# Optimization experiments

Measured on AMD Instinct MI355X. Metric: run time of the kernel, lower is better.

Reference implementation:

```python
import jax, jax.numpy as jnp
import numpy as np

NEG_SLOPE = 0.2

def _gc(inp, adj, W, b):
    # Kipf GraphConvolution: adj @ (inp @ W) + b
    return adj @ (inp @ W) + b

def _lrelu(x):
    return jnp.where(x >= 0, x, NEG_SLOPE * x)

def setup_inputs() -> dict:
    key = jax.random.key(0)
    ks = jax.random.split(key, 24)
    Nx, Ny, Fx, Fy, D1, C = 8192, 4096, 512, 256, 256, 64
    s = 0.05
    inp = {
        "hx1": jax.random.uniform(ks[0], (Nx, Nx), jnp.float32) / Nx,
        "hx2": jax.random.uniform(ks[1], (Nx, Ny), jnp.float32) / Ny,
        "x0": jax.random.normal(ks[2], (Nx, Fx), jnp.float32),
        "hy1": jax.random.uniform(ks[3], (Ny, Ny), jnp.float32) / Ny,
        "hy2": jax.random.uniform(ks[4], (Ny, Nx), jnp.float32) / Nx,
        "y0": jax.random.normal(ks[5], (Ny, Fy), jnp.float32),
        "alpha": jnp.float32(0.6),
        "beta": jnp.float32(0.4),
        # weights/biases of the 8 GraphConvolution layers
        "Wx1a": jax.random.normal(ks[6], (Fx, D1), jnp.float32) * s,
        "bx1a": jnp.zeros((D1,), jnp.float32),
        "Wx1b": jax.random.normal(ks[7], (Fy, D1), jnp.float32) * s,
        "bx1b": jnp.zeros((D1,), jnp.float32),
        "Wx2a": jax.random.normal(ks[8], (D1, C), jnp.float32) * s,
        "bx2a": jnp.zeros((C,), jnp.float32),
        "Wx2b": jax.random.normal(ks[9], (D1, C), jnp.float32) * s,
        "bx2b": jnp.zeros((C,), jnp.float32),
        "Wy1a": jax.random.normal(ks[10], (Fy, D1), jnp.float32) * s,
        "by1a": jnp.zeros((D1,), jnp.float32),
        "Wy1b": jax.random.normal(ks[11], (Fx, D1), jnp.float32) * s,
        "by1b": jnp.zeros((D1,), jnp.float32),
        "Wy2a": jax.random.normal(ks[12], (D1, C), jnp.float32) * s,
        "by2a": jnp.zeros((C,), jnp.float32),
        "Wy2b": jax.random.normal(ks[13], (D1, C), jnp.float32) * s,
        "by2b": jnp.zeros((C,), jnp.float32),
    }
    return inp

def reference(hx1, hx2, x0, hy1, hy2, y0, alpha, beta,
              Wx1a, bx1a, Wx1b, bx1b, Wx2a, bx2a, Wx2b, bx2b,
              Wy1a, by1a, Wy1b, by1b, Wy2a, by2a, Wy2b, by2b):
    # layer 1
    x1 = _lrelu(_gc(x0, hx1, Wx1a, bx1a) * alpha + _gc(y0, hx2, Wx1b, bx1b) * (1 - alpha))
    y1 = _lrelu(_gc(y0, hy1, Wy1a, by1a) * beta + _gc(x0, hy2, Wy1b, by1b) * (1 - beta))
    # layer 2
    x2 = _lrelu(_gc(x1, hx1, Wx2a, bx2a) * alpha + _gc(y1, hx2, Wx2b, bx2b) * (1 - alpha))
    y_pre = _gc(y1, hy1, Wy2a, by2a) * beta + _gc(x1, hy2, Wy2b, by2b) * (1 - beta)
    y2 = _lrelu(y_pre)
    h_hat = jax.nn.sigmoid(x2 @ y2.T)            # [Nx, Ny]
    x_output = jax.nn.log_softmax(x2, axis=1)    # [Nx, nclass]
    return (h_hat, x_output)
```

## Files before the change

### kernel.cpp

```cpp
#include <hip/hip_runtime.h>

typedef unsigned short u16;
typedef unsigned char u8;
typedef long i64;
typedef __attribute__((ext_vector_type(8))) short bf16x8;
typedef __attribute__((ext_vector_type(4))) float f32x4;
typedef __attribute__((ext_vector_type(8))) u16 u16x8;
typedef __attribute__((ext_vector_type(4))) u16 u16x4;
typedef __attribute__((ext_vector_type(4))) float f4;

#define DEVI static __device__ __forceinline__

DEVI u16 f2b(float f) { __bf16 h = (__bf16)f; return __builtin_bit_cast(u16, h); }
DEVI float b2f(u16 h) { unsigned u = ((unsigned)h) << 16; return __builtin_bit_cast(float, u); }

DEVI int pk8(float a, float b, float c, float d) {
  int w = __builtin_amdgcn_cvt_pk_fp8_f32(a, b, 0, false);
  return __builtin_amdgcn_cvt_pk_fp8_f32(c, d, w, true);
}

DEVI void gload16(const void* g, void* l) {
  __builtin_amdgcn_global_load_lds((const __attribute__((address_space(1))) void*)g,
                                   (__attribute__((address_space(3))) void*)l, 16, 0, 0);
}

__global__ __launch_bounds__(1024)
void gemmF_k(const float* __restrict__ xA0, const float* __restrict__ xA1,
             const u8* __restrict__ xB0, const u8* __restrict__ xB1,
             u8* __restrict__ xA0f8, u8* __restrict__ xA1f8,
             int xK0, int xK1, int xL0, int xL1, u16* __restrict__ xC, size_t xMN,
             const float* __restrict__ yA0, const float* __restrict__ yA1,
             const u8* __restrict__ yB0, const u8* __restrict__ yB1,
             u8* __restrict__ yA0f8, u8* __restrict__ yA1f8,
             int yK0, int yK1, int yL0, int yL1, u16* __restrict__ yC, size_t yMN)
{
  constexpr int BM = 128, BK = 64;
  constexpr int LDA = 72;
  constexpr int ASZ = BM * LDA;
  constexpr int BSZ = 256 * BK;
  constexpr int BUFSZ = ASZ + BSZ;
  constexpr float SADJ = 8192.f;
  __shared__ __align__(16) u8 lds[4 * BUFSZ];

  const int tid = threadIdx.x, lane = tid & 63, wave = tid >> 6;
  const int wm = (wave >> 2) * 32, wn = (wave & 3) * 64;
  const int lgrp = lane >> 4, lrow = lane & 15;

  const int flat = blockIdx.x;

  const float *A0, *A1; const u8 *B0, *B1; u8 *A0f8, *A1f8;
  int K0, K1, L0, L1; u16* Cout; size_t MN; int m0, z;
  if (flat < 256) {
    const int s = ((flat & 7) << 5) | (flat >> 3);
    A0=xA0; A1=xA1; B0=xB0; B1=xB1; A0f8=xA0f8; A1f8=xA1f8;
    K0=xK0; K1=xK1; L0=xL0; L1=xL1; Cout=xC; MN=xMN;
    m0 = (s & 63) * BM; z = s >> 6;
  } else {
    const int f2 = flat - 256;
    const int s = ((f2 & 7) << 5) | (f2 >> 3);
    A0=yA0; A1=yA1; B0=yB0; B1=yB1; A0f8=yA0f8; A1f8=yA1f8;
    K0=yK0; K1=yK1; L0=yL0; L1=yL1; Cout=yC; MN=yMN;
    m0 = (s & 31) * BM; z = s >> 5;
  }

  const int nt0 = L0 >> 6, NT = nt0 + (L1 >> 6);

  const int r0 = tid >> 4;
  const int cf = (tid & 15) << 2;

  f32x4 acc[2][4];
#pragma unroll
  for (int m = 0; m < 2; ++m)
#pragma unroll
    for (int n = 0; n < 4; ++n) acc[m][n] = (f32x4){0.f, 0.f, 0.f, 0.f};

  f4 rA0[2], rA1[2];

  auto tileinfo = [&](int t, const float*& Ap, const u8*& Bp, u8*& Af8, int& Kj, int& kk) {
    if (t < nt0) { Ap = A0; Bp = B0; Af8 = A0f8; Kj = K0; kk = z * L0 + (t << 6); }
    else         { Ap = A1; Bp = B1; Af8 = A1f8; Kj = K1; kk = z * L1 + ((t - nt0) << 6); }
  };

  auto loadA = [&](int t, f4 (&r)[2]) {
    const float* Ap; const u8* Bp; u8* Af8; int Kj, kk;
    tileinfo(t, Ap, Bp, Af8, Kj, kk);
#pragma unroll
    for (int j = 0; j < 2; ++j) {
      const int rr = j * 64 + r0;
      r[j] = __builtin_nontemporal_load(
          (const f4*)(Ap + (size_t)(m0 + rr) * Kj + kk + cf));
    }
  };

  auto loadB = [&](int t) {
    const float* Ap; const u8* Bp; u8* Af8; int Kj, kk;
    tileinfo(t, Ap, Bp, Af8, Kj, kk);
    u8* sB = &lds[(t & 3) * BUFSZ] + ASZ;
    const int off = tid * 16;
    const int r = off >> 6, c = off & 63;
    gload16(Bp + (size_t)r * Kj + kk + (c ^ (((r >> 1) & 3) << 4)), sB + off);
  };

  auto writeA = [&](int t, f4 (&r)[2]) {
    const float* Ap; const u8* Bp; u8* Af8; int Kj, kk;
    tileinfo(t, Ap, Bp, Af8, Kj, kk);
    u8* sA = &lds[(t & 3) * BUFSZ];
#pragma unroll
    for (int j = 0; j < 2; ++j) {
      const int rr = j * 64 + r0;
      const int pw = pk8(r[j][0] * SADJ, r[j][1] * SADJ, r[j][2] * SADJ, r[j][3] * SADJ);
      *(int*)&sA[rr * LDA + cf] = pw;
      *(int*)(Af8 + (size_t)(m0 + rr) * Kj + kk + cf) = pw;
    }
  };

  auto compute = [&](int t) {
    const u8* sA = &lds[(t & 3) * BUFSZ];
    const u8* sB = sA + ASZ;
    __builtin_amdgcn_s_setprio(1);
#pragma unroll
    for (int ks = 0; ks < 2; ++ks) {
      i64 a[2], b[4];
#pragma unroll
      for (int m = 0; m < 2; ++m) {
        const int r = wm + m * 16 + lrow;
        a[m] = *(const i64*)&sA[r * LDA + ks * 32 + lgrp * 8];
      }
#pragma unroll
      for (int n = 0; n < 4; ++n) {
        const int r = wn + n * 16 + lrow;
        b[n] = *(const i64*)&sB[r * BK + ((ks * 32 + lgrp * 8) ^ (((r >> 1) & 3) << 4))];
      }
#pragma unroll
      for (int m = 0; m < 2; ++m)
#pragma unroll
        for (int n = 0; n < 4; ++n)
          acc[m][n] = __builtin_amdgcn_mfma_f32_16x16x32_fp8_fp8(a[m], b[n], acc[m][n], 0, 0, 0);
    }
    __builtin_amdgcn_s_setprio(0);
  };

  auto step = [&](int t, f4 (&rIn)[2], f4 (&rOut)[2]) {
    const bool has_next = (t + 1 < NT);
    if (has_next) { loadA(t + 1, rOut); loadB(t + 1); }
    if (!has_next)   asm volatile("s_waitcnt vmcnt(0)" ::: "memory");
    else if (t == 0) asm volatile("s_waitcnt vmcnt(3)" ::: "memory");
    else             asm volatile("s_waitcnt vmcnt(5)" ::: "memory");
    writeA(t, rIn);
    asm volatile("s_waitcnt lgkmcnt(0)" ::: "memory");
    asm volatile("s_barrier" ::: "memory");
    compute(t);
  };

  loadA(0, rA0); loadB(0);

  for (int t = 0; t < NT; t += 2) {
    step(t, rA0, rA1);
    step(t + 1, rA1, rA0);
  }

  u16* Cp = Cout + (size_t)z * MN;
#pragma unroll
  for (int n = 0; n < 4; ++n) {
    const int c = wn + n * 16 + lrow;
#pragma unroll
    for (int m = 0; m < 2; ++m) {
      const int rb = m0 + wm + m * 16 + lgrp * 4;
#pragma unroll
      for (int q = 0; q < 4; ++q)
        Cp[(size_t)(rb + q) * 256 + c] = f2b(acc[m][n][q]);
    }
  }
}

__global__ __launch_bounds__(256)
void gemm8_k(const u8* __restrict__ xA0, const u8* __restrict__ xA1,
             const u8* __restrict__ xB0, const u8* __restrict__ xB1,
             int xK0, int xK1, int xL0, int xL1, u16* __restrict__ xC, size_t xMN,
             const u8* __restrict__ yA0, const u8* __restrict__ yA1,
             const u8* __restrict__ yB0, const u8* __restrict__ yB1,
             int yK0, int yK1, int yL0, int yL1, u16* __restrict__ yC, size_t yMN)
{
  constexpr int BM = 128, BK = 128, BN = 64;
  constexpr int MR = 4, NR = 2;
  constexpr int ASZ = BM * BK, BSZ = BN * BK;
  __shared__ __align__(16) u8 lds[3 * (ASZ + BSZ)];

  const int tid = threadIdx.x, lane = tid & 63, wave = tid >> 6;
  const int wm = (wave >> 1) * 64, wn = (wave & 1) * 32;
  const int lgrp = lane >> 4, lrow = lane & 15;

  const int flat = blockIdx.x;

  const u8 *A0, *A1, *B0, *B1; int K0, K1, L0, L1; u16* Cw; size_t MN;
  int m0, z;
  if (flat < 512) {
    const int s = ((flat & 7) << 6) | (flat >> 3);
    A0=xA0; A1=xA1; B0=xB0; B1=xB1; K0=xK0; K1=xK1; L0=xL0; L1=xL1; Cw=xC; MN=xMN;
    m0 = (s & 63) * BM; z = s >> 6;
  } else {
    const int f2 = flat - 512;
    const int s = ((f2 & 7) << 6) | (f2 >> 3);
    A0=yA0; A1=yA1; B0=yB0; B1=yB1; K0=yK0; K1=yK1; L0=yL0; L1=yL1; Cw=yC; MN=yMN;
    m0 = (s & 31) * BM; z = s >> 5;
  }

  const int nt0 = L0 >> 7, NT = nt0 + (L1 >> 7);

  f32x4 acc[MR][NR];
#pragma unroll
  for (int m = 0; m < MR; ++m)
#pragma unroll
    for (int n = 0; n < NR; ++n) acc[m][n] = (f32x4){0.f, 0.f, 0.f, 0.f};

  auto stage = [&](int buf, int t) {
    const u8* Ap; const u8* Bp; int Kj, kk;
    if (t < nt0) { Ap = A0; Bp = B0; Kj = K0; kk = z * L0 + (t << 7); }
    else         { Ap = A1; Bp = B1; Kj = K1; kk = z * L1 + ((t - nt0) << 7); }
    u8* sA = &lds[buf * (ASZ + BSZ)];
    u8* sB = sA + ASZ;
#pragma unroll
    for (int i = 0; i < ASZ / 4096; ++i) {
      const int off = i * 4096 + tid * 16;
      const int r = off >> 7, c = off & 127;
      gload16(Ap + (size_t)(m0 + r) * Kj + kk + (c ^ ((r & 7) << 4)), sA + off);
    }
#pragma unroll
    for (int i = 0; i < BSZ / 4096; ++i) {
      const int off = i * 4096 + tid * 16;
      const int r = off >> 7, c = off & 127;
      gload16(Bp + (size_t)r * Kj + kk + (c ^ ((r & 7) << 4)), sB + off);
    }
  };

  auto compute = [&](int buf) {
    const u8* sA = &lds[buf * (ASZ + BSZ)];
    const u8* sB = sA + ASZ;
    __builtin_amdgcn_s_setprio(1);
#pragma unroll
    for (int ks = 0; ks < 4; ++ks) {
      i64 a[MR], b[NR];
#pragma unroll
      for (int m = 0; m < MR; ++m) {
        const int r = wm + m * 16 + lrow;
        a[m] = *(const i64*)&sA[r * BK + ((ks * 32 + lgrp * 8) ^ ((r & 7) << 4))];
      }
#pragma unroll
      for (int n = 0; n < NR; ++n) {
        const int r = wn + n * 16 + lrow;
        b[n] = *(const i64*)&sB[r * BK + ((ks * 32 + lgrp * 8) ^ ((r & 7) << 4))];
      }
#pragma unroll
      for (int m = 0; m < MR; ++m)
#pragma unroll
        for (int n = 0; n < NR; ++n)
          acc[m][n] = __builtin_amdgcn_mfma_f32_16x16x32_fp8_fp8(a[m], b[n], acc[m][n], 0, 0, 0);
    }
    __builtin_amdgcn_s_setprio(0);
  };

  stage(0, 0);
  stage(1, 1);
  for (int t = 0; t < NT; ++t) {
    if (t + 1 < NT) asm volatile("s_waitcnt vmcnt(6)" ::: "memory");
    else            asm volatile("s_waitcnt vmcnt(0)" ::: "memory");
    asm volatile("s_barrier" ::: "memory");
    compute(t % 3);
    if (t + 2 < NT) stage((t + 2) % 3, t + 2);
  }

  u16* Cp = Cw + (size_t)z * MN;
#pragma unroll
  for (int n = 0; n < NR; ++n) {
    const int c = wn + n * 16 + lrow;
#pragma unroll
    for (int m = 0; m < MR; ++m) {
      const int rb = m0 + wm + m * 16 + lgrp * 4;
#pragma unroll
      for (int q = 0; q < 4; ++q)
        Cp[(size_t)(rb + q) * 64 + c] = f2b(acc[m][n][q]);
    }
  }
}

template<bool A_F32>
__global__ __launch_bounds__(256)
void gemmS_k(const void* Ax, const u16* Bx, int Kx, int ldcx, u8* Cx1, u8* Cx2,
             const void* Ay, const u16* By, int Ky, int ldcy, u8* Cy1, u8* Cy2,
             int ySplit, int nsplit, float sOut)
{
  constexpr int BM = 64, BN = 64, BK = 32, LD = 40;
  constexpr int MR = 2, NR = 2;
  __shared__ u16 sA[BM * LD];
  __shared__ u16 sB[BN * LD];

  const int tid  = threadIdx.x;
  const int lane = tid & 63;
  const int wave = tid >> 6;
  const int wm = (wave >> 1) * 32;
  const int wn = (wave &  1) * 32;

  const void* A0_; const u16* B0_; int K0, ldc; u8 *C1, *C2; int m0;
  if ((int)blockIdx.y < ySplit) {
    A0_ = Ax; B0_ = Bx; K0 = Kx; ldc = ldcx; C1 = Cx1; C2 = Cx2;
    m0 = blockIdx.y * BM;
  } else {
    A0_ = Ay; B0_ = By; K0 = Ky; ldc = ldcy; C1 = Cy1; C2 = Cy2;
    m0 = (blockIdx.y - ySplit) * BM;
  }
  const int n0 = blockIdx.x * BN;

  constexpr int TPRA = 256 / BM;
  constexpr int EPTA = 32 / TPRA;
  const int ar = tid / TPRA, ac = (tid % TPRA) * EPTA;
  const int br = ar, bc = ac;

  f32x4 acc[MR][NR];
#pragma unroll
  for (int m = 0; m < MR; ++m)
#pragma unroll
    for (int n = 0; n < NR; ++n) acc[m][n] = (f32x4){0.f, 0.f, 0.f, 0.f};

  const int lgrp = lane >> 4, lrow = lane & 15;

  for (int kk = 0; kk < K0; kk += BK) {
    if constexpr (A_F32) {
      const float* Ap = (const float*)A0_ + (size_t)(m0 + ar) * K0 + kk + ac;
      f4 v0 = ((const f4*)Ap)[0];
      f4 v1 = ((const f4*)Ap)[1];
      u16x8 h;
      h[0]=f2b(v0[0]); h[1]=f2b(v0[1]); h[2]=f2b(v0[2]); h[3]=f2b(v0[3]);
      h[4]=f2b(v1[0]); h[5]=f2b(v1[1]); h[6]=f2b(v1[2]); h[7]=f2b(v1[3]);
      *(u16x8*)&sA[ar * LD + ac] = h;
    } else {
      const u16* Ap = (const u16*)A0_ + (size_t)(m0 + ar) * K0 + kk + ac;
      *(u16x8*)&sA[ar * LD + ac] = *(const u16x8*)Ap;
    }
    {
      const u16* Bp = B0_ + (size_t)(n0 + br) * K0 + kk + bc;
      *(u16x8*)&sB[br * LD + bc] = *(const u16x8*)Bp;
    }
    __syncthreads();
    bf16x8 af[MR], bfr[NR];
#pragma unroll
    for (int m = 0; m < MR; ++m)
      af[m] = *(const bf16x8*)&sA[(wm + m * 16 + lrow) * LD + lgrp * 8];
#pragma unroll
    for (int n = 0; n < NR; ++n)
      bfr[n] = *(const bf16x8*)&sB[(wn + n * 16 + lrow) * LD + lgrp * 8];
#pragma unroll
    for (int m = 0; m < MR; ++m)
#pragma unroll
      for (int n = 0; n < NR; ++n)
        acc[m][n] = __builtin_amdgcn_mfma_f32_16x16x32_bf16(af[m], bfr[n], acc[m][n], 0, 0, 0);
    __syncthreads();
  }

#pragma unroll
  for (int n = 0; n < NR; ++n) {
    const int c = n0 + wn + n * 16 + lrow;
    u8* Cp = (c < nsplit) ? C1 : C2;
    const int cr = (c < nsplit) ? c : c - nsplit;
#pragma unroll
    for (int m = 0; m < MR; ++m) {
      const int rb = m0 + wm + m * 16 + lgrp * 4;
      int w = __builtin_amdgcn_cvt_pk_fp8_f32(acc[m][n][0] * sOut, acc[m][n][1] * sOut, 0, false);
      w = __builtin_amdgcn_cvt_pk_fp8_f32(acc[m][n][2] * sOut, acc[m][n][3] * sOut, w, true);
      *(int*)&Cp[(size_t)cr * ldc + rb] = w;
    }
  }
}

__global__ __launch_bounds__(256)
void gemmH_k(const u16* A0_, const u16* B0_, int K0, float* Cout, int ldc)
{
  constexpr int BM = 128, BN = 128, BK = 32, LD = 40;
  constexpr int MR = 4, NR = 4;
  __shared__ u16 sA[BM * LD];
  __shared__ u16 sB[BN * LD];

  const int tid  = threadIdx.x;
  const int lane = tid & 63;
  const int wave = tid >> 6;
  const int wm = (wave >> 1) * 64;
  const int wn = (wave &  1) * 64;
  const int m0 = blockIdx.y * BM;
  const int n0 = blockIdx.x * BN;

  constexpr int TPRA = 2;
  constexpr int EPTA = 16;
  const int ar = tid / TPRA, ac = (tid % TPRA) * EPTA;

  f32x4 acc[MR][NR];
#pragma unroll
  for (int m = 0; m < MR; ++m)
#pragma unroll
    for (int n = 0; n < NR; ++n) acc[m][n] = (f32x4){0.f, 0.f, 0.f, 0.f};

  const int lgrp = lane >> 4, lrow = lane & 15;

  for (int kk = 0; kk < K0; kk += BK) {
    {
      const u16* Ap = A0_ + (size_t)(m0 + ar) * K0 + kk + ac;
      *(u16x8*)&sA[ar * LD + ac]     = ((const u16x8*)Ap)[0];
      *(u16x8*)&sA[ar * LD + ac + 8] = ((const u16x8*)Ap)[1];
      const u16* Bp = B0_ + (size_t)(n0 + ar) * K0 + kk + ac;
      *(u16x8*)&sB[ar * LD + ac]     = ((const u16x8*)Bp)[0];
      *(u16x8*)&sB[ar * LD + ac + 8] = ((const u16x8*)Bp)[1];
    }
    __syncthreads();
    bf16x8 af[MR], bfr[NR];
#pragma unroll
    for (int m = 0; m < MR; ++m)
      af[m] = *(const bf16x8*)&sA[(wm + m * 16 + lrow) * LD + lgrp * 8];
#pragma unroll
    for (int n = 0; n < NR; ++n)
      bfr[n] = *(const bf16x8*)&sB[(wn + n * 16 + lrow) * LD + lgrp * 8];
#pragma unroll
    for (int m = 0; m < MR; ++m)
#pragma unroll
      for (int n = 0; n < NR; ++n)
        acc[m][n] = __builtin_amdgcn_mfma_f32_16x16x32_bf16(af[m], bfr[n], acc[m][n], 0, 0, 0);
    __syncthreads();
  }

  float* Cp = Cout;
#pragma unroll
  for (int n = 0; n < NR; ++n) {
    const int c = n0 + wn + n * 16 + lrow;
#pragma unroll
    for (int m = 0; m < MR; ++m) {
      const int rb = m0 + wm + m * 16 + lgrp * 4;
#pragma unroll
      for (int q = 0; q < 4; ++q)
        __builtin_nontemporal_store(1.f / (1.f + __expf(-acc[m][n][q])),
                                    &Cp[(size_t)(rb + q) * ldc + c]);
    }
  }
}

__global__ __launch_bounds__(256)
void combine1_k(const u16* __restrict__ partX, const u16* __restrict__ partY,
                int xBlocks, size_t MNx, size_t MNy, int KSx_, int KSy_,
                const float* bxa, const float* bxb, const float* ap,
                const float* bya, const float* byb, const float* bp,
                u16* x1, u16* y1, float invs)
{
  const u16* parts; size_t MN; int KS, nb, bid = blockIdx.x;
  const float *b0, *b1, *mixp; u16* out;
  if (bid < xBlocks) {
    parts = partX; MN = MNx; KS = KSx_; b0 = bxa; b1 = bxb; mixp = ap; out = x1; nb = xBlocks;
  } else {
    bid -= xBlocks;
    parts = partY; MN = MNy; KS = KSy_; b0 = bya; b1 = byb; mixp = bp; out = y1;
    nb = gridDim.x - xBlocks;
  }
  const float mix = *mixp;
  const size_t stride = (size_t)nb * 1024;
  for (size_t i = ((size_t)bid * 256 + threadIdx.x) * 4; i < MN; i += stride) {
    f4 s = {0.f, 0.f, 0.f, 0.f};
    for (int zz = 0; zz < KS; ++zz) {
      u16x4 pv = *(const u16x4*)&parts[(size_t)zz * MN + i];
#pragma unroll
      for (int q = 0; q < 4; ++q) s[q] += b2f(pv[q]);
    }
    const int c = (int)(i & 255);
    u16x4 o;
#pragma unroll
    for (int q = 0; q < 4; ++q) {
      float v = s[q] * invs + mix * b0[c + q] + (1.f - mix) * b1[c + q];
      v = v >= 0.f ? v : 0.2f * v;
      o[q] = f2b(v);
    }
    *(u16x4*)&out[i] = o;
  }
}

__global__ __launch_bounds__(256)
void combine2_k(const u16* __restrict__ partX, const u16* __restrict__ partY,
                int xRowBlocks, size_t MNx, size_t MNy,
                const float* bxa, const float* bxb, const float* ap,
                const float* bya, const float* byb, const float* bp,
                u16* x2, u16* y2, float* xout, float invs)
{
  const int w = threadIdx.x >> 6, lane = threadIdx.x & 63;
  if ((int)blockIdx.x < xRowBlocks) {
    const int row = blockIdx.x * 4 + w;
    const float a = *ap;
    float s = 0.f;
#pragma unroll
    for (int z = 0; z < 8; ++z)
      s += b2f(partX[(size_t)z * MNx + (size_t)row * 64 + lane]);
    float v = s * invs + a * bxa[lane] + (1.f - a) * bxb[lane];
    v = v >= 0.f ? v : 0.2f * v;
    x2[(size_t)row * 64 + lane] = f2b(v);
    float m = v;
#pragma unroll
    for (int o = 32; o; o >>= 1) m = fmaxf(m, __shfl_xor(m, o));
    float t = __expf(v - m);
#pragma unroll
    for (int o = 32; o; o >>= 1) t += __shfl_xor(t, o);
    xout[(size_t)row * 64 + lane] = v - m - __logf(t);
  } else {
    const int row = ((int)blockIdx.x - xRowBlocks) * 4 + w;
    const float b = *bp;
    float s = 0.f;
#pragma unroll
    for (int z = 0; z < 16; ++z)
      s += b2f(partY[(size_t)z * MNy + (size_t)row * 64 + lane]);
    float v = s * invs + b * bya[lane] + (1.f - b) * byb[lane];
    v = v >= 0.f ? v : 0.2f * v;
    y2[(size_t)row * 64 + lane] = f2b(v);
  }
}

__global__ __launch_bounds__(256)
void prep_w(const float* Wx1a, const float* Wx1b, const float* Wy1a, const float* Wy1b,
            const float* Wx2a, const float* Wx2b, const float* Wy2a, const float* Wy2b,
            u16* WtX, u16* WtY, u16* W2X, u16* W2Y,
            const float* ap, const float* bp)
{
  const int zz = blockIdx.z;
  const float a = *ap, b = *bp;
  const float* W; u16* O; int K, N, roff; float s;
  switch (zz) {
    case 0: W=Wx1a; O=WtX; K=512; N=256; roff=0;   s=a;      break;
    case 1: W=Wy1b; O=WtX; K=512; N=256; roff=256; s=1.f-b;  break;
    case 2: W=Wx1b; O=WtY; K=256; N=256; roff=0;   s=1.f-a;  break;
    case 3: W=Wy1a; O=WtY; K=256; N=256; roff=256; s=b;      break;
    case 4: W=Wx2a; O=W2X; K=256; N=64;  roff=0;   s=a;      break;
    case 5: W=Wy2b; O=W2X; K=256; N=64;  roff=64;  s=1.f-b;  break;
    case 6: W=Wx2b; O=W2Y; K=256; N=64;  roff=0;   s=1.f-a;  break;
    default:W=Wy2a; O=W2Y; K=256; N=64;  roff=64;  s=b;      break;
  }
  const int total = K * N;
  for (int i = blockIdx.x * 256 + threadIdx.x; i < total; i += gridDim.x * 256) {
    const int k = i / N, n = i - k * N;
    O[(size_t)(n + roff) * K + k] = f2b(W[i] * s);
  }
}

extern "C" void kernel_launch(void* const* d_in, const int* in_sizes, int n_in,
                              void* d_out, int out_size, void* d_ws, size_t ws_size,
                              hipStream_t stream)
{
  const float* hx1 = (const float*)d_in[0];
  const float* hx2 = (const float*)d_in[1];
  const float* x0  = (const float*)d_in[2];
  const float* hy1 = (const float*)d_in[3];
  const float* hy2 = (const float*)d_in[4];
  const float* y0  = (const float*)d_in[5];
  const float* alphap = (const float*)d_in[6];
  const float* betap  = (const float*)d_in[7];
  const float* Wx1a = (const float*)d_in[8];  const float* bx1a = (const float*)d_in[9];
  const float* Wx1b = (const float*)d_in[10]; const float* bx1b = (const float*)d_in[11];
  const float* Wx2a = (const float*)d_in[12]; const float* bx2a = (const float*)d_in[13];
  const float* Wx2b = (const float*)d_in[14]; const float* bx2b = (const float*)d_in[15];
  const float* Wy1a = (const float*)d_in[16]; const float* by1a = (const float*)d_in[17];
  const float* Wy1b = (const float*)d_in[18]; const float* by1b = (const float*)d_in[19];
  const float* Wy2a = (const float*)d_in[20]; const float* by2a = (const float*)d_in[21];
  const float* Wy2b = (const float*)d_in[22]; const float* by2b = (const float*)d_in[23];
  (void)in_sizes; (void)n_in; (void)out_size;

  constexpr int Nx = 8192, Ny = 4096, Fx = 512, Fy = 256, D1 = 256, C = 64;
  constexpr float SB1 = 16.f, SB2 = 256.f;
  constexpr float INV1 = 1.f / (8192.f * 16.f);
  constexpr float INV2 = 1.f / (8192.f * 256.f);
  constexpr int KSx = 4, KSy = 8;

  u8* wsb = (u8*)d_ws;
  size_t off = 0;
  auto alloc = [&](size_t n) { u8* p = wsb + off; off += (n + 63) & ~(size_t)63; return p; };

  u16* WtX = (u16*)alloc((size_t)512 * 512 * 2);
  u16* WtY = (u16*)alloc((size_t)512 * 256 * 2);
  u16* W2X = (u16*)alloc((size_t)128 * 256 * 2);
  u16* W2Y = (u16*)alloc((size_t)128 * 256 * 2);
  u8* B1x  = alloc((size_t)D1 * Nx);
  u8* B2x  = alloc((size_t)D1 * Ny);
  u8* B1y  = alloc((size_t)D1 * Ny);
  u8* B2y  = alloc((size_t)D1 * Nx);
  u16* x1  = (u16*)alloc((size_t)Nx * D1 * 2);
  u16* y1  = (u16*)alloc((size_t)Ny * D1 * 2);
  u8* B1x2 = alloc((size_t)C * Nx);
  u8* B2x2 = alloc((size_t)C * Ny);
  u8* B1y2 = alloc((size_t)C * Ny);
  u8* B2y2 = alloc((size_t)C * Nx);
  u16* x2  = (u16*)alloc((size_t)Nx * C * 2);
  u16* y2  = (u16*)alloc((size_t)Ny * C * 2);

  const size_t base_off = off;
  const size_t szHx1 = (size_t)Nx * Nx, szHx2 = (size_t)Nx * Ny;
  const size_t szHy1 = (size_t)Ny * Ny, szHy2 = (size_t)Ny * Nx;
  const size_t needA = base_off + szHx1 + szHx2 + szHy1 + szHy2 + ((size_t)32 << 20) + (1 << 20);

  u8 *hx1f8, *hx2f8, *hy1f8, *hy2f8; u16* part;
  if (ws_size >= needA) {
    hx1f8 = alloc(szHx1); hx2f8 = alloc(szHx2);
    hy1f8 = alloc(szHy1); hy2f8 = alloc(szHy2);
    part  = (u16*)alloc((size_t)32 << 20);
  } else {
    hy1f8 = alloc(szHy1); hy2f8 = alloc(szHy2);
    hx1f8 = (u8*)d_out;
    hx2f8 = (u8*)d_out + szHx1;
    part  = (u16*)((u8*)d_out + szHx1 + szHx2);
  }

  const size_t MNx1 = (size_t)Nx * D1, MNy1 = (size_t)Ny * D1;
  const size_t MNx2 = (size_t)Nx * C,  MNy2 = (size_t)Ny * C;
  u16* partY1 = part + (size_t)KSx * MNx1;
  u16* partY2 = part + 8 * MNx2;

  prep_w<<<dim3(256, 1, 8), 256, 0, stream>>>(Wx1a, Wx1b, Wy1a, Wy1b, Wx2a, Wx2b, Wy2a, Wy2b,
      WtX, WtY, W2X, W2Y, alphap, betap);

  gemmS_k<true><<<dim3(8, Nx/64 + Ny/64), 256, 0, stream>>>(
      x0, WtX, Fx, Nx, B1x, B2y,
      y0, WtY, Fy, Ny, B2x, B1y,
      Nx/64, 256, SB1);

  gemmF_k<<<dim3(512), 1024, 0, stream>>>(
      hx1, hx2, B1x, B2x, hx1f8, hx2f8, Nx, Ny, Nx/KSx, Ny/KSx, part, MNx1,
      hy1, hy2, B1y, B2y, hy1f8, hy2f8, Ny, Nx, Ny/KSy, Nx/KSy, partY1, MNy1);

  combine1_k<<<dim3(3072), 256, 0, stream>>>(part, partY1, 2048, MNx1, MNy1, KSx, KSy,
      bx1a, bx1b, alphap, by1a, by1b, betap, x1, y1, INV1);

  gemmS_k<false><<<dim3(2, Nx/64 + Ny/64), 256, 0, stream>>>(
      x1, W2X, D1, Nx, B1x2, B2y2,
      y1, W2Y, D1, Ny, B2x2, B1y2,
      Nx/64, 64, SB2);

  gemm8_k<<<dim3(1024), 256, 0, stream>>>(
      hx1f8, hx2f8, B1x2, B2x2, Nx, Ny, 1024, 512, part, MNx2,
      hy1f8, hy2f8, B1y2, B2y2, Ny, Nx, 256, 512, partY2, MNy2);

  combine2_k<<<dim3(2048 + 1024), 256, 0, stream>>>(part, partY2, 2048, MNx2, MNy2,
      bx2a, bx2b, alphap, by2a, by2b, betap, x2, y2,
      (float*)d_out + (size_t)Nx * Ny, INV2);

  gemmH_k<<<dim3(Ny/128, Nx/128), 256, 0, stream>>>(x2, y2, C, (float*)d_out, Ny);
}
```

Baseline: 312.0 us.

## Process two K-tiles per barrier and defer fp8 copy stores after prefetch

Restructures the main GEMM loop to convert and write two K-tiles of A into LDS per barrier, halving the number of barriers per tile. Prefetches of the next two tiles are issued right after the barrier, and the global fp8 copy of A is stored after those loads, so the stores no longer sit ahead of the vmcnt waits. This keeps more loads in flight per wave at the cost of longer register lifetimes. The vmcnt(0) wait at t==0 and the loop assume NT is even.

```diff
diff --git a/kernel.cpp b/kernel.cpp
--- a/kernel.cpp
+++ b/kernel.cpp
@@ -75,6 +75,7 @@
     for (int n = 0; n < 4; ++n) acc[m][n] = (f32x4){0.f, 0.f, 0.f, 0.f};
 
   f4 rA0[2], rA1[2];
+  int pw0[2], pw1[2];
 
   auto tileinfo = [&](int t, const float*& Ap, const u8*& Bp, u8*& Af8, int& Kj, int& kk) {
     if (t < nt0) { Ap = A0; Bp = B0; Af8 = A0f8; Kj = K0; kk = z * L0 + (t << 6); }
@@ -101,16 +102,23 @@
     gload16(Bp + (size_t)r * Kj + kk + (c ^ (((r >> 1) & 3) << 4)), sB + off);
   };
 
-  auto writeA = [&](int t, f4 (&r)[2]) {
+  auto writeLDS = [&](int t, f4 (&r)[2], int (&pw)[2]) {
+    u8* sA = &lds[(t & 3) * BUFSZ];
+#pragma unroll
+    for (int j = 0; j < 2; ++j) {
+      const int rr = j * 64 + r0;
+      pw[j] = pk8(r[j][0] * SADJ, r[j][1] * SADJ, r[j][2] * SADJ, r[j][3] * SADJ);
+      *(int*)&sA[rr * LDA + cf] = pw[j];
+    }
+  };
+
+  auto storeCopy = [&](int t, int (&pw)[2]) {
     const float* Ap; const u8* Bp; u8* Af8; int Kj, kk;
     tileinfo(t, Ap, Bp, Af8, Kj, kk);
-    u8* sA = &lds[(t & 3) * BUFSZ];
 #pragma unroll
     for (int j = 0; j < 2; ++j) {
       const int rr = j * 64 + r0;
-      const int pw = pk8(r[j][0] * SADJ, r[j][1] * SADJ, r[j][2] * SADJ, r[j][3] * SADJ);
-      *(int*)&sA[rr * LDA + cf] = pw;
-      *(int*)(Af8 + (size_t)(m0 + rr) * Kj + kk + cf) = pw;
+      *(int*)(Af8 + (size_t)(m0 + rr) * Kj + kk + cf) = pw[j];
     }
   };
 
@@ -140,23 +148,22 @@
     __builtin_amdgcn_s_setprio(0);
   };
 
-  auto step = [&](int t, f4 (&rIn)[2], f4 (&rOut)[2]) {
-    const bool has_next = (t + 1 < NT);
-    if (has_next) { loadA(t + 1, rOut); loadB(t + 1); }
-    if (!has_next)   asm volatile("s_waitcnt vmcnt(0)" ::: "memory");
-    else if (t == 0) asm volatile("s_waitcnt vmcnt(3)" ::: "memory");
-    else             asm volatile("s_waitcnt vmcnt(5)" ::: "memory");
-    writeA(t, rIn);
+  loadA(0, rA0); loadB(0);
+  loadA(1, rA1); loadB(1);
+
+  for (int t = 0; t < NT; t += 2) {
+    if (t == 0) asm volatile("s_waitcnt vmcnt(0)" ::: "memory");
+    else        asm volatile("s_waitcnt vmcnt(4)" ::: "memory");
+    writeLDS(t, rA0, pw0);
+    writeLDS(t + 1, rA1, pw1);
     asm volatile("s_waitcnt lgkmcnt(0)" ::: "memory");
     asm volatile("s_barrier" ::: "memory");
+    if (t + 2 < NT) { loadA(t + 2, rA0); loadB(t + 2); }
+    if (t + 3 < NT) { loadA(t + 3, rA1); loadB(t + 3); }
+    storeCopy(t, pw0);
+    storeCopy(t + 1, pw1);
     compute(t);
-  };
-
-  loadA(0, rA0); loadB(0);
-
-  for (int t = 0; t < NT; t += 2) {
-    step(t, rA0, rA1);
-    step(t + 1, rA1, rA0);
+    compute(t + 1);
   }
 
   u16* Cp = Cout + (size_t)z * MN;
```

Measured after the change: 305.3 us (median of 2 runs). 1.02x faster.
